# Kernel optimization log

Measured on AMD Instinct MI355X. Metric: run time of the kernel, lower is better.

Reference implementation:

```python
import jax, jax.numpy as jnp
import numpy as np

B, N, E, DIN, DOUT = 8, 4096, 160, 15, 15


def _mha(q, k, v, in_w, in_b, out_w, out_b, h):
    # torch.nn.MultiheadAttention math: packed in_proj, per-head scaled dot attn, out_proj.
    e = q.shape[-1]
    d = e // h
    scale = 1.0 / np.sqrt(d)

    def proj(x, w, b):
        y = x @ w.T + b
        return jnp.moveaxis(y.reshape(y.shape[:-1] + (h, d)), -2, -3)  # [..., h, L, d]

    qh = proj(q, in_w[:e], in_b[:e])
    kh = proj(k, in_w[e:2 * e], in_b[e:2 * e])
    vh = proj(v, in_w[2 * e:], in_b[2 * e:])
    a = jax.nn.softmax(jnp.einsum('...hld,...hmd->...hlm', qh, kh) * scale, axis=-1)
    o = jnp.einsum('...hlm,...hmd->...hld', a, vh)
    o = jnp.moveaxis(o, -3, -2).reshape(q.shape)
    return o @ out_w.T + out_b


def _attn_layer(seq, Wq, Wk, Wv, in_w, in_b, out_w, out_b, h):
    # AttentionLayer: extra Wq/Wk/Wv projections feeding the MHA
    return _mha(seq @ Wq, seq @ Wk, seq @ Wv, in_w, in_b, out_w, out_b, h)


def setup_inputs():
    key = jax.random.key(0)
    ks = jax.random.split(key, 20)
    s = 1.0 / np.sqrt(E)
    p = lambda i, shape: jax.random.normal(ks[i], shape, dtype=jnp.float32) * s
    return {
        'X_batch': jax.random.normal(ks[0], (B, N, E), dtype=jnp.float32),
        'in_idx': jax.random.randint(ks[1], (B, N, DIN), 0, N),
        'out_idx': jax.random.randint(ks[2], (B, N, DOUT), 0, N),
        'iWq': p(3, (E, E)), 'iWk': p(4, (E, E)), 'iWv': p(5, (E, E)),
        'i_in_w': p(6, (3 * E, E)), 'i_in_b': jnp.zeros(3 * E, jnp.float32),
        'i_out_w': p(7, (E, E)), 'i_out_b': jnp.zeros(E, jnp.float32),
        'oWq': p(8, (E, E)), 'oWk': p(9, (E, E)), 'oWv': p(10, (E, E)),
        'o_in_w': p(11, (3 * E, E)), 'o_in_b': jnp.zeros(3 * E, jnp.float32),
        'o_out_w': p(12, (E, E)), 'o_out_b': jnp.zeros(E, jnp.float32),
        'f_in_w': p(13, (3 * E, E)), 'f_in_b': jnp.zeros(3 * E, jnp.float32),
        'f_out_w': p(14, (E, E)), 'f_out_b': jnp.zeros(E, jnp.float32),
        'lin_w': p(15, (E, E)), 'lin_b': jnp.zeros(E, jnp.float32),
    }


def reference(X_batch, in_idx, out_idx,
              iWq, iWk, iWv, i_in_w, i_in_b, i_out_w, i_out_b,
              oWq, oWk, oWv, o_in_w, o_in_b, o_out_w, o_out_b,
              f_in_w, f_in_b, f_out_w, f_out_b, lin_w, lin_b):
    b_ix = jnp.arange(X_batch.shape[0])[:, None, None]
    self_f = X_batch[:, :, None, :]                                   # [B,N,1,E]
    seq_in = jnp.concatenate([self_f, X_batch[b_ix, in_idx]], axis=2)  # [B,N,1+DIN,E]
    seq_out = jnp.concatenate([self_f, X_batch[b_ix, out_idx]], axis=2)
    a_in = _attn_layer(seq_in, iWq, iWk, iWv, i_in_w, i_in_b, i_out_w, i_out_b, 5)
    a_out = _attn_layer(seq_out, oWq, oWk, oWv, o_in_w, o_in_b, o_out_w, o_out_b, 5)
    a = jnp.concatenate([a_in, a_out], axis=2)                         # [B,N,2+DIN+DOUT,E]
    f = _mha(a, a, a, f_in_w, f_in_b, f_out_w, f_out_b, 1)
    pooled = jnp.max(f, axis=2)                                        # max over sequence dim
    return jax.nn.elu(pooled @ lin_w.T + lin_b)
```

## Files before the change

### kernel.cpp

```cpp
#include <hip/hip_runtime.h>
#include <hip/hip_bf16.h>
#include <math.h>

#define NTH 256

typedef __bf16 bf16x8 __attribute__((ext_vector_type(8)));
typedef float  f32x4  __attribute__((ext_vector_type(4)));
typedef unsigned short ushort;
typedef ushort u16x8 __attribute__((ext_vector_type(8)));

__device__ __forceinline__ ushort f2bf(float x){
    union { __bf16 b; ushort u; } v;
    v.b = (__bf16)x;
    return v.u;
}
__device__ __forceinline__ float bf2f(ushort h){
    union { unsigned int u; float f; } v; v.u = ((unsigned int)h) << 16;
    return v.f;
}

__global__ void prep_combined_bf(const float* __restrict__ Wq, const float* __restrict__ Wk,
                                 const float* __restrict__ Wv, const float* __restrict__ in_w,
                                 ushort* __restrict__ dh)
{
    int o = blockIdx.x*NTH + threadIdx.x;
    if (o >= 76800) return;
    int c = o/160, j = o - c*160;
    const float* Wsel = (c<160) ? Wq : (c<320) ? Wk : Wv;
    const float* wrow = Wsel + j*160;
    const float* irow = in_w + c*160;
    float s = 0.f;
    for (int k=0;k<160;k++) s = fmaf(wrow[k], irow[k], s);
    dh[o] = f2bf(s);
}

__global__ void prep_H_split(const float* __restrict__ f_in_w, const float* __restrict__ out_w,
                             ushort* __restrict__ dh, float* __restrict__ tmp)
{
    int o = blockIdx.x*NTH + threadIdx.x;
    if (o >= 76800) return;
    int n = o/160, k = o - n*160;
    float s = 0.f;
    for (int c=0;c<160;c++) s = fmaf(f_in_w[n*160+c], out_w[c*160+k], s);
    if (n < 320) dh[o] = f2bf(s);
    else         tmp[(n-320)*160 + k] = s;
}

__global__ void prep_H_fold(const float* __restrict__ fo, const float* __restrict__ Hv,
                            ushort* __restrict__ dh)
{
    int o = blockIdx.x*NTH + threadIdx.x;
    if (o >= 25600) return;
    int n = o/160, k = o - n*160;
    float s = 0.f;
    for (int j=0;j<160;j++) s = fmaf(fo[n*160+j], Hv[j*160+k], s);
    dh[(320+n)*160 + k] = f2bf(s);
}

__global__ void prep_cvec(const float* __restrict__ f_in_w, const float* __restrict__ out_b,
                          const float* __restrict__ f_in_b, float* __restrict__ cvt)
{
    int n = blockIdx.x*NTH + threadIdx.x;
    if (n >= 480) return;
    float s = f_in_b[n];
    for (int c=0;c<160;c++) s = fmaf(f_in_w[n*160+c], out_b[c], s);
    cvt[n] = s;
}

__global__ void prep_cvec_fold(const float* __restrict__ fo, const float* __restrict__ cvt,
                               float* __restrict__ cv)
{
    int n = blockIdx.x*NTH + threadIdx.x;
    if (n >= 480) return;
    if (n < 320){ cv[n] = cvt[n]; return; }
    int m = n - 320;
    float s = 0.f;
    for (int j=0;j<160;j++) s = fmaf(fo[m*160+j], cvt[320+j], s);
    cv[n] = s;
}

__global__ void prep_conv_bf1(const float* __restrict__ src, ushort* __restrict__ dh, int n)
{
    int o = blockIdx.x*NTH + threadIdx.x;
    if (o >= n) return;
    dh[o] = f2bf(src[o]);
}

__global__ void prep_conv_bf2(const float* __restrict__ src,
                              ushort* __restrict__ dh, ushort* __restrict__ dl, int n)
{
    int o = blockIdx.x*NTH + threadIdx.x;
    if (o >= n) return;
    float s = src[o];
    ushort h = f2bf(s);
    dh[o] = h; dl[o] = f2bf(s - bf2f(h));
}

__global__ __launch_bounds__(NTH)
void gemm_mfma_lin(const float* __restrict__ A,
                   const ushort* __restrict__ Wh, const ushort* __restrict__ Wl,
                   const float* __restrict__ bias, float* __restrict__ C, int N)
{
    __shared__ ushort sAh[128*40], sAl[128*40];
    __shared__ ushort sWh[160*40], sWl[160*40];

    const int tid = threadIdx.x;
    const int lane = tid & 63, wave = tid >> 6;
    const int wm = wave >> 1, wn = wave & 1;
    const int ln = lane & 15, g = lane >> 4;
    const long m0 = (long)blockIdx.x * 128;
    const int  n0 = blockIdx.y * 160;

    f32x4 acc[4][5];
#pragma unroll
    for (int mt=0;mt<4;mt++)
#pragma unroll
        for (int nt=0;nt<5;nt++)
#pragma unroll
            for (int r=0;r<4;r++) acc[mt][nt][r] = 0.f;

    for (int k0=0;k0<160;k0+=32){
#pragma unroll
        for (int i=0;i<4;i++){
            int f = tid + 256*i;
            int m = f >> 3, seg = f & 7;
            float4 v = *(const float4*)(A + (m0+m)*160 + k0 + seg*4);
            ushort4 hv, lv;
            hv.x = f2bf(v.x); lv.x = f2bf(v.x - bf2f(hv.x));
            hv.y = f2bf(v.y); lv.y = f2bf(v.y - bf2f(hv.y));
            hv.z = f2bf(v.z); lv.z = f2bf(v.z - bf2f(hv.z));
            hv.w = f2bf(v.w); lv.w = f2bf(v.w - bf2f(hv.w));
            *(ushort4*)(sAh + m*40 + seg*4) = hv;
            *(ushort4*)(sAl + m*40 + seg*4) = lv;
        }
#pragma unroll
        for (int i=0;i<5;i++){
            int e = tid + 256*i;
            int pl = (e >= 640);
            int idx = pl ? e-640 : e;
            int n = idx >> 2, seg = idx & 3;
            const ushort* src = (pl ? Wl : Wh) + (long)(n0+n)*160 + k0 + seg*8;
            ushort* dst = (pl ? sWl : sWh) + n*40 + seg*8;
            *(uint4*)dst = *(const uint4*)src;
        }
        __syncthreads();

        bf16x8 ah[4], al[4];
#pragma unroll
        for (int mt=0;mt<4;mt++){
            int off = (wm*64 + mt*16 + ln)*40 + g*8;
            ah[mt] = *(const bf16x8*)(sAh + off);
            al[mt] = *(const bf16x8*)(sAl + off);
        }
#pragma unroll
        for (int nt=0;nt<5;nt++){
            int offw = (wn*80 + nt*16 + ln)*40 + g*8;
            bf16x8 bh = *(const bf16x8*)(sWh + offw);
            bf16x8 bl = *(const bf16x8*)(sWl + offw);
#pragma unroll
            for (int mt=0;mt<4;mt++){
                acc[mt][nt] = __builtin_amdgcn_mfma_f32_16x16x32_bf16(ah[mt], bh, acc[mt][nt], 0,0,0);
                acc[mt][nt] = __builtin_amdgcn_mfma_f32_16x16x32_bf16(al[mt], bh, acc[mt][nt], 0,0,0);
                acc[mt][nt] = __builtin_amdgcn_mfma_f32_16x16x32_bf16(ah[mt], bl, acc[mt][nt], 0,0,0);
            }
        }
        __syncthreads();
    }

#pragma unroll
    for (int nt=0;nt<5;nt++){
        int col = n0 + wn*80 + nt*16 + ln;
        float bv = bias[col];
#pragma unroll
        for (int mt=0;mt<4;mt++){
#pragma unroll
            for (int r=0;r<4;r++){
                long row = m0 + wm*64 + mt*16 + g*4 + r;
                float x = acc[mt][nt][r] + bv;
                x = x > 0.f ? x : expm1f(x);
                C[row*N + col] = x;
            }
        }
    }
}

__global__ __launch_bounds__(NTH)
void gemm_bf(const ushort* __restrict__ A0, const ushort* __restrict__ A1,
             const ushort* __restrict__ Wh0, const ushort* __restrict__ Wh1,
             const float* __restrict__ b0, const float* __restrict__ b1,
             ushort* __restrict__ C0, ushort* __restrict__ C1, int N)
{
    const int z = blockIdx.z;
    const ushort* A  = z ? A1 : A0;
    const ushort* Wh = z ? Wh1 : Wh0;
    const float* bias = z ? b1 : b0;
    ushort* C = z ? C1 : C0;

    __shared__ ushort sA[128*40];
    __shared__ ushort sW[160*40];

    const int tid = threadIdx.x;
    const int lane = tid & 63, wave = tid >> 6;
    const int wm = wave >> 1, wn = wave & 1;
    const int ln = lane & 15, g = lane >> 4;
    const long m0 = (long)blockIdx.x * 128;
    const int  n0 = blockIdx.y * 160;

    f32x4 acc[4][5];
#pragma unroll
    for (int mt=0;mt<4;mt++)
#pragma unroll
        for (int nt=0;nt<5;nt++)
#pragma unroll
            for (int r=0;r<4;r++) acc[mt][nt][r] = 0.f;

    for (int k0=0;k0<160;k0+=32){
#pragma unroll
        for (int i=0;i<2;i++){
            int e = tid + 256*i;
            int m = e >> 2, seg = e & 3;
            *(uint4*)(sA + m*40 + seg*8) =
                *(const uint4*)(A + (m0+m)*160 + k0 + seg*8);
        }
#pragma unroll
        for (int i=0;i<3;i++){
            int e = tid + 256*i;
            if (e < 640){
                int n = e >> 2, seg = e & 3;
                *(uint4*)(sW + n*40 + seg*8) =
                    *(const uint4*)(Wh + (long)(n0+n)*160 + k0 + seg*8);
            }
        }
        __syncthreads();

        bf16x8 af[4];
#pragma unroll
        for (int mt=0;mt<4;mt++)
            af[mt] = *(const bf16x8*)(sA + (wm*64 + mt*16 + ln)*40 + g*8);
#pragma unroll
        for (int nt=0;nt<5;nt++){
            bf16x8 bh = *(const bf16x8*)(sW + (wn*80 + nt*16 + ln)*40 + g*8);
#pragma unroll
            for (int mt=0;mt<4;mt++)
                acc[mt][nt] = __builtin_amdgcn_mfma_f32_16x16x32_bf16(af[mt], bh, acc[mt][nt], 0,0,0);
        }
        __syncthreads();
    }

#pragma unroll
    for (int nt=0;nt<5;nt++){
        int col = n0 + wn*80 + nt*16 + ln;
        float bv = bias[col];
#pragma unroll
        for (int mt=0;mt<4;mt++){
#pragma unroll
            for (int r=0;r<4;r++){
                long row = m0 + wm*64 + mt*16 + g*4 + r;
                C[row*N + col] = f2bf(acc[mt][nt][r] + bv);
            }
        }
    }
}

#define XST 504
__global__ __launch_bounds__(512)
void mega_node(const ushort* __restrict__ XPi, const ushort* __restrict__ XPo,
               const int* __restrict__ in_idx, const int* __restrict__ out_idx,
               const ushort* __restrict__ Hi, const ushort* __restrict__ Ho,
               const float* __restrict__ c_i, const float* __restrict__ c_o,
               const float* __restrict__ fb, float* __restrict__ pooled)
{
    __shared__ ushort lds[36352];

    const int tid  = threadIdx.x;
    const int lane = tid & 63, w = tid >> 6;
    const int ln = lane & 15, g = lane >> 4;
    const int bid = ((int)blockIdx.x & 7) * 2048 + ((int)blockIdx.x >> 3);
    const int nl0 = bid * 2;

    ushort* XPg = lds;
    ushort* sO  = lds + 16128;
    ushort* sPh = lds + 26880;

    const int ndA = w & 1, p = w >> 1;
    const int nodeA = nl0 + ndA;
    const int bb = nodeA >> 12, nn = nodeA & 4095;
    int idx0 = nn, idx1 = nn;
    if (lane >= 1 && lane < 16){
        idx0 = in_idx [(long)nodeA*15 + lane-1];
        idx1 = out_idx[(long)nodeA*15 + lane-1];
    }

#pragma unroll
    for (int i=0;i<4;i++){
        int e = i*256 + p*64 + lane;
        if (e < 960){
            int r = e/60, c = e - r*60;
            int rowg = __shfl(idx0, r);
            *(uint4*)(XPg + ndA*16*XST + r*XST + c*8) =
                *(const uint4*)(XPi + (long)(bb*4096 + rowg)*480 + c*8);
        }
    }
    __syncthreads();

    const float scale1 = 0.17677669529663687f;
#pragma unroll
    for (int l=0; l<2; l++){
        if (l == 1){
#pragma unroll
            for (int i=0;i<4;i++){
                int e = i*256 + p*64 + lane;
                if (e < 960){
                    int r = e/60, c = e - r*60;
                    int rowg = __shfl(idx1, r);
                    *(uint4*)(XPg + ndA*16*XST + r*XST + c*8) =
                        *(const uint4*)(XPo + (long)(bb*4096 + rowg)*480 + c*8);
                }
            }
            __syncthreads();
        }

#pragma unroll
        for (int rep=0; rep<2; rep++){
            int t = w + rep*8;
            if (t < 10){
                int nd = t/5, h = t - 5*(t/5);
                const ushort* xg = XPg + nd*16*XST;

                bf16x8 ka = *(const bf16x8*)(xg + ln*XST + 160 + h*32 + g*8);
                bf16x8 qb = *(const bf16x8*)(xg + ln*XST +       h*32 + g*8);
                f32x4 s = {0.f,0.f,0.f,0.f};
                __builtin_amdgcn_s_setprio(1);
                s = __builtin_amdgcn_mfma_f32_16x16x32_bf16(ka, qb, s, 0,0,0);
                __builtin_amdgcn_s_setprio(0);
                float x[4], m = -1e30f;
#pragma unroll
                for (int r=0;r<4;r++){ x[r] = s[r]*scale1; m = fmaxf(m, x[r]); }
                m = fmaxf(m, __shfl_xor(m, 16));
                m = fmaxf(m, __shfl_xor(m, 32));
                float e0[4], sum = 0.f;
#pragma unroll
                for (int r=0;r<4;r++){ e0[r] = __expf(x[r]-m); sum += e0[r]; }
                sum += __shfl_xor(sum, 16);
                sum += __shfl_xor(sum, 32);
                float inv = 1.f/sum;
                ushort4 pw;
                pw.x = f2bf(e0[0]*inv); pw.y = f2bf(e0[1]*inv);
                pw.z = f2bf(e0[2]*inv); pw.w = f2bf(e0[3]*inv);
                *(ushort4*)(sPh + t*384 + ln*24 + g*4) = pw;

                u16x8 ta;
#pragma unroll
                for (int jj=0;jj<8;jj++) ta[jj] = 0;
                if (g < 2) ta = *(const u16x8*)(sPh + t*384 + ln*24 + g*8);
                bf16x8 ap = *(bf16x8*)&ta;
#pragma unroll
                for (int half=0; half<2; half++){
                    u16x8 tb;
#pragma unroll
                    for (int jj=0;jj<8;jj++) tb[jj] = 0;
                    if (g < 2){
#pragma unroll
                        for (int jj=0;jj<8;jj++)
                            tb[jj] = xg[(g*8+jj)*XST + 320 + h*32 + half*16 + ln];
                    }
                    bf16x8 bv = *(bf16x8*)&tb;
                    f32x4 o = {0.f,0.f,0.f,0.f};
                    __builtin_amdgcn_s_setprio(1);
                    o = __builtin_amdgcn_mfma_f32_16x16x32_bf16(ap, bv, o, 0,0,0);
                    __builtin_amdgcn_s_setprio(0);
#pragma unroll
                    for (int r=0;r<4;r++)
                        sO[((nd*2+l)*16 + g*4+r)*168 + h*32 + half*16 + ln] = f2bf(o[r]);
                }
            }
        }
        __syncthreads();
    }

    const int wl = w >> 2, wn = w & 3;
    const ushort* Hw = wl ? Ho  : Hi;
    const float*  cw = wl ? c_o : c_i;

    bf16x8 ofr[2][5];
#pragma unroll
    for (int nd=0; nd<2; nd++)
#pragma unroll
        for (int kc=0; kc<5; kc++)
            ofr[nd][kc] = *(const bf16x8*)(sO + ((nd*2+wl)*16 + ln)*168 + kc*32 + g*8);

    bf16x8 hf[5], hn[5];
#pragma unroll
    for (int kc=0; kc<5; kc++)
        hf[kc] = *(const bf16x8*)(Hw + (long)(wn*16 + ln)*160 + kc*32 + g*8);
    __syncthreads();

    ushort* sFQ = lds;
    ushort* sVt = lds + 20992;
    ushort* sPf = lds + 33792;

    for (int t=0; t<8; t++){
        const int cg = t*4 + wn;
        if (t < 7){
            const int cgn = cg + 4;
            if (cgn < 30){
                const ushort* hrow = Hw + (long)(cgn*16 + ln)*160;
#pragma unroll
                for (int kc=0; kc<5; kc++)
                    hn[kc] = *(const bf16x8*)(hrow + kc*32 + g*8);
            }
        }

        if (cg < 30){
            f32x4 acc[2];
#pragma unroll
            for (int nd=0; nd<2; nd++)
#pragma unroll
                for (int r=0;r<4;r++) acc[nd][r] = 0.f;

            __builtin_amdgcn_s_setprio(1);
#pragma unroll
            for (int kc=0; kc<5; kc++)
#pragma unroll
                for (int nd=0; nd<2; nd++)
                    acc[nd] = __builtin_amdgcn_mfma_f32_16x16x32_bf16(hf[kc], ofr[nd][kc], acc[nd], 0,0,0);
            __builtin_amdgcn_s_setprio(0);

            const int cb0 = cg*16 + g*4;
            float4 cb = *(const float4*)(cw + cb0);
            if (cg < 20){
#pragma unroll
                for (int nd=0; nd<2; nd++){
                    ushort4 w4;
                    w4.x = f2bf(acc[nd][0] + cb.x);
                    w4.y = f2bf(acc[nd][1] + cb.y);
                    w4.z = f2bf(acc[nd][2] + cb.z);
                    w4.w = f2bf(acc[nd][3] + cb.w);
                    *(ushort4*)(sFQ + nd*10496 + (wl*16 + ln)*328 + cb0) = w4;
                }
            } else {
                const int c0 = cb0 - 320;
#pragma unroll
                for (int nd=0; nd<2; nd++){
                    sVt[nd*6400 + (c0+0)*40 + wl*16 + ln] = f2bf(acc[nd][0] + cb.x);
                    sVt[nd*6400 + (c0+1)*40 + wl*16 + ln] = f2bf(acc[nd][1] + cb.y);
                    sVt[nd*6400 + (c0+2)*40 + wl*16 + ln] = f2bf(acc[nd][2] + cb.z);
                    sVt[nd*6400 + (c0+3)*40 + wl*16 + ln] = f2bf(acc[nd][3] + cb.w);
                }
            }
        }
#pragma unroll
        for (int kc=0; kc<5; kc++) hf[kc] = hn[kc];
    }
    __syncthreads();

    const int nd = w >> 1, th = w & 1;
    const ushort* myQ = sFQ + nd*10496;
    const ushort* myV = sVt + nd*6400;
    ushort*       myP = sPf + nd*1280;

    if (w < 4){
        f32x4 sc[2];
#pragma unroll
        for (int tj=0; tj<2; tj++){
            f32x4 a = {0.f,0.f,0.f,0.f};
            __builtin_amdgcn_s_setprio(1);
#pragma unroll
            for (int kc=0; kc<5; kc++){
                bf16x8 ka = *(const bf16x8*)(myQ + (tj*16+ln)*328 + 160 + kc*32 + g*8);
                bf16x8 qb = *(const bf16x8*)(myQ + (th*16+ln)*328 +       kc*32 + g*8);
                a = __builtin_amdgcn_mfma_f32_16x16x32_bf16(ka, qb, a, 0,0,0);
            }
            __builtin_amdgcn_s_setprio(0);
            sc[tj] = a;
        }

        const float scale = 0.07905694150420949f;
        float x[2][4], m = -1e30f;
#pragma unroll
        for (int tj=0; tj<2; tj++)
#pragma unroll
            for (int r=0;r<4;r++){ x[tj][r] = sc[tj][r]*scale; m = fmaxf(m, x[tj][r]); }
        m = fmaxf(m, __shfl_xor(m, 16));
        m = fmaxf(m, __shfl_xor(m, 32));
        float sum = 0.f;
#pragma unroll
        for (int tj=0; tj<2; tj++)
#pragma unroll
            for (int r=0;r<4;r++){ x[tj][r] = __expf(x[tj][r]-m); sum += x[tj][r]; }
        sum += __shfl_xor(sum, 16);
        sum += __shfl_xor(sum, 32);
        float inv = 1.f/sum;
#pragma unroll
        for (int tj=0; tj<2; tj++){
            ushort4 pw;
            pw.x = f2bf(x[tj][0]*inv); pw.y = f2bf(x[tj][1]*inv);
            pw.z = f2bf(x[tj][2]*inv); pw.w = f2bf(x[tj][3]*inv);
            *(ushort4*)(myP + (th*16+ln)*40 + tj*16 + g*4) = pw;
        }
    }
    __syncthreads();

    if (w < 4){
        bf16x8 ap[2];
#pragma unroll
        for (int mi=0; mi<2; mi++)
            ap[mi] = *(const bf16x8*)(myP + (mi*16+ln)*40 + g*8);

        const long node = (long)nl0 + nd;
#pragma unroll
        for (int nt5=0; nt5<5; nt5++){
            const int nt = th*5 + nt5;
            bf16x8 bv = *(const bf16x8*)(myV + (nt*16+ln)*40 + g*8);
            float vmax = -1e30f;
            __builtin_amdgcn_s_setprio(1);
            f32x4 o0 = {0.f,0.f,0.f,0.f}, o1 = {0.f,0.f,0.f,0.f};
            o0 = __builtin_amdgcn_mfma_f32_16x16x32_bf16(ap[0], bv, o0, 0,0,0);
            o1 = __builtin_amdgcn_mfma_f32_16x16x32_bf16(ap[1], bv, o1, 0,0,0);
            __builtin_amdgcn_s_setprio(0);
#pragma unroll
            for (int r=0;r<4;r++) vmax = fmaxf(vmax, fmaxf(o0[r], o1[r]));
            vmax = fmaxf(vmax, __shfl_xor(vmax, 16));
            vmax = fmaxf(vmax, __shfl_xor(vmax, 32));
            if (g == 0){
                int col = nt*16 + ln;
                pooled[node*160 + col] = vmax + fb[col];
            }
        }
    }
}

extern "C" void kernel_launch(void* const* d_in, const int* in_sizes, int n_in,
                              void* d_out, int out_size, void* d_ws, size_t ws_size,
                              hipStream_t stream)
{
    const float* X       = (const float*)d_in[0];
    const int*   in_idx  = (const int*)  d_in[1];
    const int*   out_idx = (const int*)  d_in[2];
    const float* iWq     = (const float*)d_in[3];
    const float* iWk     = (const float*)d_in[4];
    const float* iWv     = (const float*)d_in[5];
    const float* i_in_w  = (const float*)d_in[6];
    const float* i_in_b  = (const float*)d_in[7];
    const float* i_out_w = (const float*)d_in[8];
    const float* i_out_b = (const float*)d_in[9];
    const float* oWq     = (const float*)d_in[10];
    const float* oWk     = (const float*)d_in[11];
    const float* oWv     = (const float*)d_in[12];
    const float* o_in_w  = (const float*)d_in[13];
    const float* o_in_b  = (const float*)d_in[14];
    const float* o_out_w = (const float*)d_in[15];
    const float* o_out_b = (const float*)d_in[16];
    const float* f_in_w  = (const float*)d_in[17];
    const float* f_in_b  = (const float*)d_in[18];
    const float* f_out_w = (const float*)d_in[19];
    const float* f_out_b = (const float*)d_in[20];
    const float* lin_w   = (const float*)d_in[21];
    const float* lin_b   = (const float*)d_in[22];

    float* ws = (float*)d_ws;
    float* pooled = ws;
    float* c_i    = pooled + 5242880;
    float* c_o    = c_i + 480;
    float* cvt_i  = c_o + 480;
    float* cvt_o  = cvt_i + 480;
    float* Hvt_i  = cvt_o + 480;
    float* Hvt_o  = Hvt_i + 25600;
    ushort* Xb    = (ushort*)(Hvt_o + 25600);
    ushort* XPb_i = Xb + 5242880;
    ushort* XPb_o = XPb_i + 15728640;
    ushort* Wci_h = XPb_o + 15728640;
    ushort* Wco_h = Wci_h + 76800;
    ushort* Hi_h  = Wco_h + 76800;
    ushort* Ho_h  = Hi_h  + 76800;
    ushort* li_h  = Ho_h  + 76800;
    ushort* li_l  = li_h  + 25600;

    prep_combined_bf<<<300,NTH,0,stream>>>(iWq,iWk,iWv,i_in_w, Wci_h);
    prep_combined_bf<<<300,NTH,0,stream>>>(oWq,oWk,oWv,o_in_w, Wco_h);
    prep_H_split<<<300,NTH,0,stream>>>(f_in_w, i_out_w, Hi_h, Hvt_i);
    prep_H_split<<<300,NTH,0,stream>>>(f_in_w, o_out_w, Ho_h, Hvt_o);
    prep_H_fold<<<100,NTH,0,stream>>>(f_out_w, Hvt_i, Hi_h);
    prep_H_fold<<<100,NTH,0,stream>>>(f_out_w, Hvt_o, Ho_h);
    prep_cvec<<<2,NTH,0,stream>>>(f_in_w, i_out_b, f_in_b, cvt_i);
    prep_cvec<<<2,NTH,0,stream>>>(f_in_w, o_out_b, f_in_b, cvt_o);
    prep_cvec_fold<<<2,NTH,0,stream>>>(f_out_w, cvt_i, c_i);
    prep_cvec_fold<<<2,NTH,0,stream>>>(f_out_w, cvt_o, c_o);
    prep_conv_bf2<<<100,NTH,0,stream>>>(lin_w, li_h, li_l, 25600);
    prep_conv_bf1<<<20480,NTH,0,stream>>>(X, Xb, 5242880);

    dim3 g1(256, 3, 2);
    gemm_bf<<<g1,NTH,0,stream>>>(Xb, Xb, Wci_h, Wco_h, i_in_b, o_in_b,
                                 XPb_i, XPb_o, 480);

    mega_node<<<16384,512,0,stream>>>(XPb_i, XPb_o, in_idx, out_idx,
                                      Hi_h, Ho_h, c_i, c_o, f_out_b, pooled);

    dim3 g6(256, 1);
    gemm_mfma_lin<<<g6,NTH,0,stream>>>(pooled, li_h, li_l, lin_b, (float*)d_out, 160);
}
```

Baseline: 802.3 us.

## Process one node per 256-thread block instead of two per 512-thread block

The per-node fused attention kernel now handles a single node per block with 4 waves, using half the LDS, and launches twice as many blocks. All per-node indexing is simplified and the s_setprio hints around MFMAs are removed. This aims to raise occupancy and cut synchronization cost per block, but it gives up sharing H weight fragments across two nodes, so the H matrix is loaded from global/cache twice as often per node. Each wave now does more sequential iterations of the H projection loop.

```diff
diff --git a/kernel.cpp b/kernel.cpp
--- a/kernel.cpp
+++ b/kernel.cpp
@@ -263,41 +263,38 @@
 }
 
 #define XST 504
-__global__ __launch_bounds__(512)
+__global__ __launch_bounds__(NTH)
 void mega_node(const ushort* __restrict__ XPi, const ushort* __restrict__ XPo,
                const int* __restrict__ in_idx, const int* __restrict__ out_idx,
                const ushort* __restrict__ Hi, const ushort* __restrict__ Ho,
                const float* __restrict__ c_i, const float* __restrict__ c_o,
                const float* __restrict__ fb, float* __restrict__ pooled)
 {
-    __shared__ ushort lds[36352];
+    __shared__ ushort lds[18176];
 
     const int tid  = threadIdx.x;
     const int lane = tid & 63, w = tid >> 6;
     const int ln = lane & 15, g = lane >> 4;
-    const int bid = ((int)blockIdx.x & 7) * 2048 + ((int)blockIdx.x >> 3);
-    const int nl0 = bid * 2;
+    const int node = ((int)blockIdx.x & 7) * 4096 + ((int)blockIdx.x >> 3);
 
     ushort* XPg = lds;
-    ushort* sO  = lds + 16128;
-    ushort* sPh = lds + 26880;
-
-    const int ndA = w & 1, p = w >> 1;
-    const int nodeA = nl0 + ndA;
-    const int bb = nodeA >> 12, nn = nodeA & 4095;
+    ushort* sO  = lds + 8064;
+    ushort* sPh = lds + 13440;
+
+    const int bb = node >> 12, nn = node & 4095;
     int idx0 = nn, idx1 = nn;
     if (lane >= 1 && lane < 16){
-        idx0 = in_idx [(long)nodeA*15 + lane-1];
-        idx1 = out_idx[(long)nodeA*15 + lane-1];
+        idx0 = in_idx [(long)node*15 + lane-1];
+        idx1 = out_idx[(long)node*15 + lane-1];
     }
 
 #pragma unroll
     for (int i=0;i<4;i++){
-        int e = i*256 + p*64 + lane;
+        int e = i*256 + tid;
         if (e < 960){
             int r = e/60, c = e - r*60;
             int rowg = __shfl(idx0, r);
-            *(uint4*)(XPg + ndA*16*XST + r*XST + c*8) =
+            *(uint4*)(XPg + r*XST + c*8) =
                 *(const uint4*)(XPi + (long)(bb*4096 + rowg)*480 + c*8);
         }
     }
@@ -309,11 +306,11 @@
         if (l == 1){
 #pragma unroll
             for (int i=0;i<4;i++){
-                int e = i*256 + p*64 + lane;
+                int e = i*256 + tid;
                 if (e < 960){
                     int r = e/60, c = e - r*60;
                     int rowg = __shfl(idx1, r);
-                    *(uint4*)(XPg + ndA*16*XST + r*XST + c*8) =
+                    *(uint4*)(XPg + r*XST + c*8) =
                         *(const uint4*)(XPo + (long)(bb*4096 + rowg)*480 + c*8);
                 }
             }
@@ -322,17 +319,12 @@
 
 #pragma unroll
         for (int rep=0; rep<2; rep++){
-            int t = w + rep*8;
-            if (t < 10){
-                int nd = t/5, h = t - 5*(t/5);
-                const ushort* xg = XPg + nd*16*XST;
-
-                bf16x8 ka = *(const bf16x8*)(xg + ln*XST + 160 + h*32 + g*8);
-                bf16x8 qb = *(const bf16x8*)(xg + ln*XST +       h*32 + g*8);
+            int h = w + rep*4;
+            if (h < 5){
+                bf16x8 ka = *(const bf16x8*)(XPg + ln*XST + 160 + h*32 + g*8);
+                bf16x8 qb = *(const bf16x8*)(XPg + ln*XST +       h*32 + g*8);
                 f32x4 s = {0.f,0.f,0.f,0.f};
-                __builtin_amdgcn_s_setprio(1);
                 s = __builtin_amdgcn_mfma_f32_16x16x32_bf16(ka, qb, s, 0,0,0);
-                __builtin_amdgcn_s_setprio(0);
                 float x[4], m = -1e30f;
 #pragma unroll
                 for (int r=0;r<4;r++){ x[r] = s[r]*scale1; m = fmaxf(m, x[r]); }
@@ -347,12 +339,12 @@
                 ushort4 pw;
                 pw.x = f2bf(e0[0]*inv); pw.y = f2bf(e0[1]*inv);
                 pw.z = f2bf(e0[2]*inv); pw.w = f2bf(e0[3]*inv);
-                *(ushort4*)(sPh + t*384 + ln*24 + g*4) = pw;
+                *(ushort4*)(sPh + h*384 + ln*24 + g*4) = pw;
 
                 u16x8 ta;
 #pragma unroll
                 for (int jj=0;jj<8;jj++) ta[jj] = 0;
-                if (g < 2) ta = *(const u16x8*)(sPh + t*384 + ln*24 + g*8);
+                if (g < 2) ta = *(const u16x8*)(sPh + h*384 + ln*24 + g*8);
                 bf16x8 ap = *(bf16x8*)&ta;
 #pragma unroll
                 for (int half=0; half<2; half++){
@@ -362,32 +354,28 @@
                     if (g < 2){
 #pragma unroll
                         for (int jj=0;jj<8;jj++)
-                            tb[jj] = xg[(g*8+jj)*XST + 320 + h*32 + half*16 + ln];
+                            tb[jj] = XPg[(g*8+jj)*XST + 320 + h*32 + half*16 + ln];
                     }
                     bf16x8 bv = *(bf16x8*)&tb;
                     f32x4 o = {0.f,0.f,0.f,0.f};
-                    __builtin_amdgcn_s_setprio(1);
                     o = __builtin_amdgcn_mfma_f32_16x16x32_bf16(ap, bv, o, 0,0,0);
-                    __builtin_amdgcn_s_setprio(0);
 #pragma unroll
                     for (int r=0;r<4;r++)
-                        sO[((nd*2+l)*16 + g*4+r)*168 + h*32 + half*16 + ln] = f2bf(o[r]);
+                        sO[(l*16 + g*4+r)*168 + h*32 + half*16 + ln] = f2bf(o[r]);
                 }
             }
         }
         __syncthreads();
     }
 
-    const int wl = w >> 2, wn = w & 3;
+    const int wl = w >> 1, wn = w & 1;
     const ushort* Hw = wl ? Ho  : Hi;
     const float*  cw = wl ? c_o : c_i;
 
-    bf16x8 ofr[2][5];
-#pragma unroll
-    for (int nd=0; nd<2; nd++)
-#pragma unroll
-        for (int kc=0; kc<5; kc++)
-            ofr[nd][kc] = *(const bf16x8*)(sO + ((nd*2+wl)*16 + ln)*168 + kc*32 + g*8);
+    bf16x8 ofr[5];
+#pragma unroll
+    for (int kc=0; kc<5; kc++)
+        ofr[kc] = *(const bf16x8*)(sO + (wl*16 + ln)*168 + kc*32 + g*8);
 
     bf16x8 hf[5], hn[5];
 #pragma unroll
@@ -396,82 +384,56 @@
     __syncthreads();
 
     ushort* sFQ = lds;
-    ushort* sVt = lds + 20992;
-    ushort* sPf = lds + 33792;
-
-    for (int t=0; t<8; t++){
-        const int cg = t*4 + wn;
-        if (t < 7){
-            const int cgn = cg + 4;
-            if (cgn < 30){
-                const ushort* hrow = Hw + (long)(cgn*16 + ln)*160;
-#pragma unroll
-                for (int kc=0; kc<5; kc++)
-                    hn[kc] = *(const bf16x8*)(hrow + kc*32 + g*8);
-            }
-        }
-
-        if (cg < 30){
-            f32x4 acc[2];
-#pragma unroll
-            for (int nd=0; nd<2; nd++)
-#pragma unroll
-                for (int r=0;r<4;r++) acc[nd][r] = 0.f;
-
-            __builtin_amdgcn_s_setprio(1);
+    ushort* sVt = lds + 10496;
+    ushort* sPf = lds + 16896;
+
+    for (int t=0; t<15; t++){
+        const int cg = t*2 + wn;
+        if (t < 14){
+            const ushort* hrow = Hw + (long)((cg+2)*16 + ln)*160;
 #pragma unroll
             for (int kc=0; kc<5; kc++)
-#pragma unroll
-                for (int nd=0; nd<2; nd++)
-                    acc[nd] = __builtin_amdgcn_mfma_f32_16x16x32_bf16(hf[kc], ofr[nd][kc], acc[nd], 0,0,0);
-            __builtin_amdgcn_s_setprio(0);
-
-            const int cb0 = cg*16 + g*4;
-            float4 cb = *(const float4*)(cw + cb0);
-            if (cg < 20){
-#pragma unroll
-                for (int nd=0; nd<2; nd++){
-                    ushort4 w4;
-                    w4.x = f2bf(acc[nd][0] + cb.x);
-                    w4.y = f2bf(acc[nd][1] + cb.y);
-                    w4.z = f2bf(acc[nd][2] + cb.z);
-                    w4.w = f2bf(acc[nd][3] + cb.w);
-                    *(ushort4*)(sFQ + nd*10496 + (wl*16 + ln)*328 + cb0) = w4;
-                }
-            } else {
-                const int c0 = cb0 - 320;
-#pragma unroll
-                for (int nd=0; nd<2; nd++){
-                    sVt[nd*6400 + (c0+0)*40 + wl*16 + ln] = f2bf(acc[nd][0] + cb.x);
-                    sVt[nd*6400 + (c0+1)*40 + wl*16 + ln] = f2bf(acc[nd][1] + cb.y);
-                    sVt[nd*6400 + (c0+2)*40 + wl*16 + ln] = f2bf(acc[nd][2] + cb.z);
-                    sVt[nd*6400 + (c0+3)*40 + wl*16 + ln] = f2bf(acc[nd][3] + cb.w);
-                }
-            }
+                hn[kc] = *(const bf16x8*)(hrow + kc*32 + g*8);
+        }
+
+        f32x4 acc = {0.f,0.f,0.f,0.f};
+#pragma unroll
+        for (int kc=0; kc<5; kc++)
+            acc = __builtin_amdgcn_mfma_f32_16x16x32_bf16(hf[kc], ofr[kc], acc, 0,0,0);
+
+        const int cb0 = cg*16 + g*4;
+        float4 cb = *(const float4*)(cw + cb0);
+        if (cg < 20){
+            ushort4 w4;
+            w4.x = f2bf(acc[0] + cb.x);
+            w4.y = f2bf(acc[1] + cb.y);
+            w4.z = f2bf(acc[2] + cb.z);
+            w4.w = f2bf(acc[3] + cb.w);
+            *(ushort4*)(sFQ + (wl*16 + ln)*328 + cb0) = w4;
+        } else {
+            const int c0 = cb0 - 320;
+            sVt[(c0+0)*40 + wl*16 + ln] = f2bf(acc[0] + cb.x);
+            sVt[(c0+1)*40 + wl*16 + ln] = f2bf(acc[1] + cb.y);
+            sVt[(c0+2)*40 + wl*16 + ln] = f2bf(acc[2] + cb.z);
+            sVt[(c0+3)*40 + wl*16 + ln] = f2bf(acc[3] + cb.w);
         }
 #pragma unroll
         for (int kc=0; kc<5; kc++) hf[kc] = hn[kc];
     }
     __syncthreads();
 
-    const int nd = w >> 1, th = w & 1;
-    const ushort* myQ = sFQ + nd*10496;
-    const ushort* myV = sVt + nd*6400;
-    ushort*       myP = sPf + nd*1280;
-
-    if (w < 4){
+    const int th = w;
+    if (w < 2){
         f32x4 sc[2];
 #pragma unroll
         for (int tj=0; tj<2; tj++){
             f32x4 a = {0.f,0.f,0.f,0.f};
-            __builtin_amdgcn_s_setprio(1);
 #pragma unroll
             for (int kc=0; kc<5; kc++){
-                bf16x8 ka = *(const bf16x8*)(myQ + (tj*16+ln)*328 + 160 + kc*32 + g*8);
-                bf16x8 qb = *(const bf16x8*)(myQ + (th*16+ln)*328 +       kc*32 + g*8);
+                bf16x8 ka = *(const bf16x8*)(sFQ + (tj*16+ln)*328 + 160 + kc*32 + g*8);
+                bf16x8 qb = *(const bf16x8*)(sFQ + (th*16+ln)*328 +       kc*32 + g*8);
                 a = __builtin_amdgcn_mfma_f32_16x16x32_bf16(ka, qb, a, 0,0,0);
             }
-            __builtin_amdgcn_s_setprio(0);
             sc[tj] = a;
         }
 
@@ -496,35 +458,32 @@
             ushort4 pw;
             pw.x = f2bf(x[tj][0]*inv); pw.y = f2bf(x[tj][1]*inv);
             pw.z = f2bf(x[tj][2]*inv); pw.w = f2bf(x[tj][3]*inv);
-            *(ushort4*)(myP + (th*16+ln)*40 + tj*16 + g*4) = pw;
+            *(ushort4*)(sPf + (th*16+ln)*40 + tj*16 + g*4) = pw;
         }
     }
     __syncthreads();
 
-    if (w < 4){
+    if (w < 2){
         bf16x8 ap[2];
 #pragma unroll
         for (int mi=0; mi<2; mi++)
-            ap[mi] = *(const bf16x8*)(myP + (mi*16+ln)*40 + g*8);
-
-        const long node = (long)nl0 + nd;
+            ap[mi] = *(const bf16x8*)(sPf + (mi*16+ln)*40 + g*8);
+
 #pragma unroll
         for (int nt5=0; nt5<5; nt5++){
             const int nt = th*5 + nt5;
-            bf16x8 bv = *(const bf16x8*)(myV + (nt*16+ln)*40 + g*8);
+            bf16x8 bv = *(const bf16x8*)(sVt + (nt*16+ln)*40 + g*8);
             float vmax = -1e30f;
-            __builtin_amdgcn_s_setprio(1);
             f32x4 o0 = {0.f,0.f,0.f,0.f}, o1 = {0.f,0.f,0.f,0.f};
             o0 = __builtin_amdgcn_mfma_f32_16x16x32_bf16(ap[0], bv, o0, 0,0,0);
             o1 = __builtin_amdgcn_mfma_f32_16x16x32_bf16(ap[1], bv, o1, 0,0,0);
-            __builtin_amdgcn_s_setprio(0);
 #pragma unroll
             for (int r=0;r<4;r++) vmax = fmaxf(vmax, fmaxf(o0[r], o1[r]));
             vmax = fmaxf(vmax, __shfl_xor(vmax, 16));
             vmax = fmaxf(vmax, __shfl_xor(vmax, 32));
             if (g == 0){
                 int col = nt*16 + ln;
-                pooled[node*160 + col] = vmax + fb[col];
+                pooled[(long)node*160 + col] = vmax + fb[col];
             }
         }
     }
@@ -593,7 +552,7 @@
     gemm_bf<<<g1,NTH,0,stream>>>(Xb, Xb, Wci_h, Wco_h, i_in_b, o_in_b,
                                  XPb_i, XPb_o, 480);
 
-    mega_node<<<16384,512,0,stream>>>(XPb_i, XPb_o, in_idx, out_idx,
+    mega_node<<<32768,NTH,0,stream>>>(XPb_i, XPb_o, in_idx, out_idx,
                                       Hi_h, Ho_h, c_i, c_o, f_out_b, pooled);
 
     dim3 g6(256, 1);
```

Result: slower. 947.5 us (+18.1%).
